# Optimization experiments

Hardware: AMD Instinct MI355X
Metric: run time of the kernel (lower is better)

## Reference

```python
import jax, jax.numpy as jnp
import numpy as np
import math

MSG_DIM = 128
ATT_DIM = 128
N = 20000
KN = 32  # neighbors per node


def setup_inputs() -> dict:
    key = jax.random.key(0)
    ks = jax.random.split(key, 8)
    s = 1.0 / math.sqrt(MSG_DIM)
    return {
        "query_msg": jax.random.normal(ks[0], (N, MSG_DIM), dtype=jnp.float32),
        "neighbor_msgs": jax.random.normal(ks[1], (N, KN, MSG_DIM), dtype=jnp.float32),
        # nn.Linear params: weight [out, in], bias [out]
        "Wq": jax.random.uniform(ks[2], (ATT_DIM, MSG_DIM), jnp.float32, -s, s),
        "bq": jax.random.uniform(ks[3], (ATT_DIM,), jnp.float32, -s, s),
        "Wk": jax.random.uniform(ks[4], (ATT_DIM, MSG_DIM), jnp.float32, -s, s),
        "bk": jax.random.uniform(ks[5], (ATT_DIM,), jnp.float32, -s, s),
        "Wv": jax.random.uniform(ks[6], (MSG_DIM, MSG_DIM), jnp.float32, -s, s),
        "bv": jax.random.uniform(ks[7], (MSG_DIM,), jnp.float32, -s, s),
    }


def reference(query_msg, neighbor_msgs, Wq, bq, Wk, bk, Wv, bv):
    scale = math.sqrt(ATT_DIM)
    Q = query_msg @ Wq.T + bq                       # [N, att_dim]
    K = jnp.einsum('nkd,ad->nka', neighbor_msgs, Wk) + bk  # [N, K, att_dim]
    V = jnp.einsum('nkd,md->nkm', neighbor_msgs, Wv) + bv  # [N, K, msg_dim]
    scores = jnp.einsum('na,nka->nk', Q, K) / scale  # [N, K]
    att = jax.nn.softmax(scores, axis=1)             # softmax over neighbors
    return jnp.einsum('nk,nkm->nm', att, V)          # [N, msg_dim]
```

## Files before the change

### kernel.cpp

```cpp
#include <hip/hip_runtime.h>
#include <math.h>

#define MSG 128
#define KN 32

__global__ void gac_prep(const float* __restrict__ Wq, const float* __restrict__ bq,
                         const float* __restrict__ Wk,
                         float* __restrict__ Mp, float* __restrict__ cp) {
    const float inv_scale = 0.088388347648318440f;
    const int d = blockIdx.x;
    const int e = threadIdx.x;
    float acc = 0.f;
#pragma unroll 8
    for (int a = 0; a < 128; ++a)
        acc = fmaf(Wk[a * 128 + d], Wq[a * 128 + e], acc);
    Mp[d * 128 + e] = acc * inv_scale;

    if (threadIdx.x < 64) {
        const int l = threadIdx.x;
        float p = Wk[l * 128 + d] * bq[l] + Wk[(l + 64) * 128 + d] * bq[l + 64];
#pragma unroll
        for (int off = 32; off; off >>= 1) p += __shfl_down(p, off, 64);
        if (l == 0) cp[d] = p * inv_scale;
    }
}

__global__ __launch_bounds__(256, 2)
void gac_main(const float* __restrict__ query,
              const float* __restrict__ nbr,
              const float* __restrict__ Mp,
              const float* __restrict__ cp,
              const float* __restrict__ Wv,
              const float* __restrict__ bv,
              float* __restrict__ out,
              int N, int npb) {
    __shared__ __align__(16) float qbuf[128];
    __shared__ __align__(16) float q2[128];
    __shared__ __align__(16) float part[2][128];
    __shared__ __align__(16) float partw[4][128];
    __shared__ float scores_s[32];
    __shared__ float att_s[32];
    __shared__ __align__(16) float ctx2[128];

    const int t = threadIdx.x;
    const int r = t & 127;
    const int h = t >> 7;
    const int w = t >> 6;
    const int l = t & 63;

    float4 wA[16], wV[16];
    {
        const float4* a = (const float4*)(Mp + r * 128 + h * 64);
        const float4* v = (const float4*)(Wv + r * 128 + h * 64);
#pragma unroll
        for (int i = 0; i < 16; ++i) { wA[i] = a[i]; wV[i] = v[i]; }
    }
    const float c_r  = (h == 0) ? cp[r] : 0.f;
    const float bv_r = (h == 0) ? bv[r] : 0.f;

    const int n0 = blockIdx.x * npb;
    const int n1 = min(n0 + npb, N);
    if (n0 >= n1) return;

    float2 xv[8];
    {
        const float* x = nbr + (size_t)n0 * KN * MSG;
#pragma unroll
        for (int j = 0; j < 8; ++j)
            xv[j] = ((const float2*)(x + (w + 4 * j) * MSG))[l];
    }

    for (int n = n0; n < n1; ++n) {
        if (t < 32)
            ((float4*)qbuf)[t] = ((const float4*)(query + (size_t)n * MSG))[t];
        __syncthreads();

        float acc = c_r;
        {
            const float4* q4 = (const float4*)(qbuf + h * 64);
#pragma unroll
            for (int i = 0; i < 16; ++i) {
                float4 qv = q4[i];
                acc = fmaf(wA[i].x, qv.x, acc);
                acc = fmaf(wA[i].y, qv.y, acc);
                acc = fmaf(wA[i].z, qv.z, acc);
                acc = fmaf(wA[i].w, qv.w, acc);
            }
        }
        part[h][r] = acc;
        __syncthreads();
        if (t < 128) q2[t] = part[0][t] + part[1][t];
        __syncthreads();

        const float2 qq = ((const float2*)q2)[l];
#pragma unroll
        for (int j = 0; j < 8; ++j) {
            float p = xv[j].x * qq.x + xv[j].y * qq.y;
#pragma unroll
            for (int off = 32; off; off >>= 1) p += __shfl_down(p, off, 64);
            if (l == 0) scores_s[w + 4 * j] = p;
        }
        __syncthreads();

        if (t < 32) {
            float s = scores_s[t];
            float m = s;
#pragma unroll
            for (int off = 16; off; off >>= 1) m = fmaxf(m, __shfl_xor(m, off, 64));
            float e = __expf(s - m);
            float sum = e;
#pragma unroll
            for (int off = 16; off; off >>= 1) sum += __shfl_xor(sum, off, 64);
            att_s[t] = e / sum;
        }
        __syncthreads();

        float2 pc = make_float2(0.f, 0.f);
#pragma unroll
        for (int j = 0; j < 8; ++j) {
            float a = att_s[w + 4 * j];
            pc.x = fmaf(a, xv[j].x, pc.x);
            pc.y = fmaf(a, xv[j].y, pc.y);
        }
        ((float2*)partw[w])[l] = pc;

        if (n + 1 < n1) {
            const float* x = nbr + (size_t)(n + 1) * KN * MSG;
#pragma unroll
            for (int j = 0; j < 8; ++j)
                xv[j] = ((const float2*)(x + (w + 4 * j) * MSG))[l];
        }
        __syncthreads();
        if (t < 128) ctx2[t] = partw[0][t] + partw[1][t] + partw[2][t] + partw[3][t];
        __syncthreads();

        float acco = bv_r;
        {
            const float4* c4 = (const float4*)(ctx2 + h * 64);
#pragma unroll
            for (int i = 0; i < 16; ++i) {
                float4 cv = c4[i];
                acco = fmaf(wV[i].x, cv.x, acco);
                acco = fmaf(wV[i].y, cv.y, acco);
                acco = fmaf(wV[i].z, cv.z, acco);
                acco = fmaf(wV[i].w, cv.w, acco);
            }
        }
        part[h][r] = acco;
        __syncthreads();
        if (t < 128) out[(size_t)n * MSG + t] = part[0][t] + part[1][t];
    }
}

extern "C" void kernel_launch(void* const* d_in, const int* in_sizes, int n_in,
                              void* d_out, int out_size, void* d_ws, size_t ws_size,
                              hipStream_t stream) {
    const float* query = (const float*)d_in[0];
    const float* nbr   = (const float*)d_in[1];
    const float* Wq    = (const float*)d_in[2];
    const float* bq    = (const float*)d_in[3];
    const float* Wk    = (const float*)d_in[4];
    const float* Wv    = (const float*)d_in[6];
    const float* bv    = (const float*)d_in[7];
    float* out = (float*)d_out;

    float* Mp = (float*)d_ws;
    float* cp = Mp + 128 * 128;

    const int N = in_sizes[0] / MSG;

    gac_prep<<<128, 128, 0, stream>>>(Wq, bq, Wk, Mp, cp);

    const int npb = 40;
    const int grid = (N + npb - 1) / npb;
    gac_main<<<grid, 256, 0, stream>>>(query, nbr, Mp, cp, Wv, bv, out, N, npb);
}
```

Measured before the change: 524.8 us.

## Split fused attention kernel into batched matvec and per-wave attention kernels

Replaces the single persistent kernel, which looped over nodes with many block-level barriers per node, with three launches. A batched matvec kernel projects 16 queries per block through the folded Wq/Wk matrix. An attention kernel then gives each wave one node, holds all 32 neighbor rows in registers, and uses only wave shuffles. A second matvec applies Wv to the context vectors. This removes per-node __syncthreads and serialized small matvecs and reuses each weight register across 16 rows, at the cost of extra global round trips for Q and ctx and three extra launches.

```diff
diff --git a/kernel.cpp b/kernel.cpp
--- a/kernel.cpp
+++ b/kernel.cpp
@@ -26,130 +26,103 @@
 }
 
 __global__ __launch_bounds__(256, 2)
-void gac_main(const float* __restrict__ query,
-              const float* __restrict__ nbr,
-              const float* __restrict__ Mp,
-              const float* __restrict__ cp,
-              const float* __restrict__ Wv,
-              const float* __restrict__ bv,
-              float* __restrict__ out,
-              int N, int npb) {
-    __shared__ __align__(16) float qbuf[128];
-    __shared__ __align__(16) float q2[128];
-    __shared__ __align__(16) float part[2][128];
-    __shared__ __align__(16) float partw[4][128];
-    __shared__ float scores_s[32];
-    __shared__ float att_s[32];
-    __shared__ __align__(16) float ctx2[128];
-
+void gac_matvec16(const float* __restrict__ in, const float* __restrict__ W,
+                  const float* __restrict__ b, float* __restrict__ out, int N) {
+    __shared__ __align__(16) float qs[16 * 128];
+    __shared__ __align__(16) float part[2 * 16 * 128];
     const int t = threadIdx.x;
     const int r = t & 127;
     const int h = t >> 7;
+
+    float4 wreg[16];
+    {
+        const float4* wp = (const float4*)(W + r * 128 + h * 64);
+#pragma unroll
+        for (int i = 0; i < 16; ++i) wreg[i] = wp[i];
+    }
+    const float br = (h == 0) ? b[r] : 0.f;
+
+    const int n0 = blockIdx.x * 16;
+    const size_t maxf4 = (size_t)N * (MSG / 4) - 1;
+    {
+        const float4* src = (const float4*)in;
+        size_t i0 = (size_t)n0 * 32 + t;
+        size_t i1 = i0 + 256;
+        ((float4*)qs)[t]       = src[i0 > maxf4 ? maxf4 : i0];
+        ((float4*)qs)[t + 256] = src[i1 > maxf4 ? maxf4 : i1];
+    }
+    __syncthreads();
+
+    float acc[16];
+#pragma unroll
+    for (int j = 0; j < 16; ++j) acc[j] = br;
+#pragma unroll
+    for (int i = 0; i < 16; ++i) {
+        const float4 w4 = wreg[i];
+#pragma unroll
+        for (int j = 0; j < 16; ++j) {
+            const float4 q4 = ((const float4*)(qs + j * 128 + h * 64))[i];
+            acc[j] = fmaf(w4.x, q4.x, acc[j]);
+            acc[j] = fmaf(w4.y, q4.y, acc[j]);
+            acc[j] = fmaf(w4.z, q4.z, acc[j]);
+            acc[j] = fmaf(w4.w, q4.w, acc[j]);
+        }
+    }
+#pragma unroll
+    for (int j = 0; j < 16; ++j) part[h * 2048 + j * 128 + r] = acc[j];
+    __syncthreads();
+
+#pragma unroll
+    for (int i = 0; i < 8; ++i) {
+        const int e = t + 256 * i;
+        const int n = n0 + (e >> 7);
+        if (n < N) out[(size_t)n0 * MSG + e] = part[e] + part[2048 + e];
+    }
+}
+
+__global__ __launch_bounds__(256, 4)
+void gac_attn(const float* __restrict__ Qpp, const float* __restrict__ nbr,
+              float* __restrict__ ctx, int N) {
+    const int t = threadIdx.x;
     const int w = t >> 6;
     const int l = t & 63;
+    const int n = blockIdx.x * 4 + w;
+    if (n >= N) return;
 
-    float4 wA[16], wV[16];
-    {
-        const float4* a = (const float4*)(Mp + r * 128 + h * 64);
-        const float4* v = (const float4*)(Wv + r * 128 + h * 64);
+    const float* x = nbr + (size_t)n * KN * MSG;
+    float2 xv[KN];
 #pragma unroll
-        for (int i = 0; i < 16; ++i) { wA[i] = a[i]; wV[i] = v[i]; }
-    }
-    const float c_r  = (h == 0) ? cp[r] : 0.f;
-    const float bv_r = (h == 0) ? bv[r] : 0.f;
+    for (int k = 0; k < KN; ++k)
+        xv[k] = ((const float2*)(x + k * MSG))[l];
+    const float2 qq = ((const float2*)(Qpp + (size_t)n * MSG))[l];
 
-    const int n0 = blockIdx.x * npb;
-    const int n1 = min(n0 + npb, N);
-    if (n0 >= n1) return;
-
-    float2 xv[8];
-    {
-        const float* x = nbr + (size_t)n0 * KN * MSG;
+    float s = 0.f;
+    const int myk = l & 31;
 #pragma unroll
-        for (int j = 0; j < 8; ++j)
-            xv[j] = ((const float2*)(x + (w + 4 * j) * MSG))[l];
+    for (int k = 0; k < KN; ++k) {
+        float p = fmaf(xv[k].y, qq.y, xv[k].x * qq.x);
+#pragma unroll
+        for (int off = 32; off; off >>= 1) p += __shfl_xor(p, off, 64);
+        if (myk == k) s = p;
     }
 
-    for (int n = n0; n < n1; ++n) {
-        if (t < 32)
-            ((float4*)qbuf)[t] = ((const float4*)(query + (size_t)n * MSG))[t];
-        __syncthreads();
+    float m = s;
+#pragma unroll
+    for (int off = 16; off; off >>= 1) m = fmaxf(m, __shfl_xor(m, off, 64));
+    const float e = __expf(s - m);
+    float sum = e;
+#pragma unroll
+    for (int off = 16; off; off >>= 1) sum += __shfl_xor(sum, off, 64);
+    const float a = e / sum;
 
-        float acc = c_r;
-        {
-            const float4* q4 = (const float4*)(qbuf + h * 64);
+    float2 c = make_float2(0.f, 0.f);
 #pragma unroll
-            for (int i = 0; i < 16; ++i) {
-                float4 qv = q4[i];
-                acc = fmaf(wA[i].x, qv.x, acc);
-                acc = fmaf(wA[i].y, qv.y, acc);
-                acc = fmaf(wA[i].z, qv.z, acc);
-                acc = fmaf(wA[i].w, qv.w, acc);
-            }
-        }
-        part[h][r] = acc;
-        __syncthreads();
-        if (t < 128) q2[t] = part[0][t] + part[1][t];
-        __syncthreads();
-
-        const float2 qq = ((const float2*)q2)[l];
-#pragma unroll
-        for (int j = 0; j < 8; ++j) {
-            float p = xv[j].x * qq.x + xv[j].y * qq.y;
-#pragma unroll
-            for (int off = 32; off; off >>= 1) p += __shfl_down(p, off, 64);
-            if (l == 0) scores_s[w + 4 * j] = p;
-        }
-        __syncthreads();
-
-        if (t < 32) {
-            float s = scores_s[t];
-            float m = s;
-#pragma unroll
-            for (int off = 16; off; off >>= 1) m = fmaxf(m, __shfl_xor(m, off, 64));
-            float e = __expf(s - m);
-            float sum = e;
-#pragma unroll
-            for (int off = 16; off; off >>= 1) sum += __shfl_xor(sum, off, 64);
-            att_s[t] = e / sum;
-        }
-        __syncthreads();
-
-        float2 pc = make_float2(0.f, 0.f);
-#pragma unroll
-        for (int j = 0; j < 8; ++j) {
-            float a = att_s[w + 4 * j];
-            pc.x = fmaf(a, xv[j].x, pc.x);
-            pc.y = fmaf(a, xv[j].y, pc.y);
-        }
-        ((float2*)partw[w])[l] = pc;
-
-        if (n + 1 < n1) {
-            const float* x = nbr + (size_t)(n + 1) * KN * MSG;
-#pragma unroll
-            for (int j = 0; j < 8; ++j)
-                xv[j] = ((const float2*)(x + (w + 4 * j) * MSG))[l];
-        }
-        __syncthreads();
-        if (t < 128) ctx2[t] = partw[0][t] + partw[1][t] + partw[2][t] + partw[3][t];
-        __syncthreads();
-
-        float acco = bv_r;
-        {
-            const float4* c4 = (const float4*)(ctx2 + h * 64);
-#pragma unroll
-            for (int i = 0; i < 16; ++i) {
-                float4 cv = c4[i];
-                acco = fmaf(wV[i].x, cv.x, acco);
-                acco = fmaf(wV[i].y, cv.y, acco);
-                acco = fmaf(wV[i].z, cv.z, acco);
-                acco = fmaf(wV[i].w, cv.w, acco);
-            }
-        }
-        part[h][r] = acco;
-        __syncthreads();
-        if (t < 128) out[(size_t)n * MSG + t] = part[0][t] + part[1][t];
+    for (int k = 0; k < KN; ++k) {
+        const float ak = __shfl(a, k, 64);
+        c.x = fmaf(ak, xv[k].x, c.x);
+        c.y = fmaf(ak, xv[k].y, c.y);
     }
+    ((float2*)(ctx + (size_t)n * MSG))[l] = c;
 }
 
 extern "C" void kernel_launch(void* const* d_in, const int* in_sizes, int n_in,
@@ -164,14 +137,20 @@
     const float* bv    = (const float*)d_in[7];
     float* out = (float*)d_out;
 
-    float* Mp = (float*)d_ws;
-    float* cp = Mp + 128 * 128;
+    const int N = in_sizes[0] / MSG;
 
-    const int N = in_sizes[0] / MSG;
+    float* Mp   = (float*)d_ws;
+    float* cp   = Mp + 128 * 128;
+    float* Qpp  = cp + 128;
+    float* ctxb = Qpp + (size_t)N * MSG;
 
     gac_prep<<<128, 128, 0, stream>>>(Wq, bq, Wk, Mp, cp);
 
-    const int npb = 40;
-    const int grid = (N + npb - 1) / npb;
-    gac_main<<<grid, 256, 0, stream>>>(query, nbr, Mp, cp, Wv, bv, out, N, npb);
+    const int gmv = (N + 15) / 16;
+    gac_matvec16<<<gmv, 256, 0, stream>>>(query, Mp, cp, Qpp, N);
+
+    const int gat = (N + 3) / 4;
+    gac_attn<<<gat, 256, 0, stream>>>(Qpp, nbr, ctxb, N);
+
+    gac_matvec16<<<gmv, 256, 0, stream>>>(ctxb, Wv, bv, out, N);
 }
```

Measured after the change: 502.5 us. 1.04x faster.
